# Optimization experiments

Hardware: AMD Instinct MI355X
Metric: run time of the kernel (lower is better)

Reference implementation:

```python
import jax, jax.numpy as jnp
import numpy as np

TOP_K = 2
ROUTED_SCALING = 1.0


def setup_inputs() -> dict:
    key = jax.random.key(0)
    k1, k2, k3, k4 = jax.random.split(key, 4)
    S, B, H = 1024, 2, 1024
    E, FFN = 8, 1408
    return {
        "hidden_states": jax.random.normal(k1, (S, B, H), dtype=jnp.float32),
        "gate_w": jax.random.normal(k2, (E, H), dtype=jnp.float32) * 0.02,
        "w1": jax.random.normal(k3, (E, H, 2 * FFN), dtype=jnp.float32) * 0.02,
        "w2": jax.random.normal(k4, (E, FFN, H), dtype=jnp.float32) * 0.02,
    }


def reference(hidden_states, gate_w, w1, w2):
    # hidden_states: [S, B, H] -> transpose(0,1) as in MoELayer.forward
    x = jnp.transpose(hidden_states, (1, 0, 2))  # [B, S, H]
    B, S, H = x.shape
    E = gate_w.shape[0]
    xt = x.reshape(-1, H)  # [T, H], T = B*S
    T = xt.shape[0]

    # --- TopKGate ('greedy', softmax scoring) ---
    scores = jax.nn.softmax(xt @ gate_w.T, axis=-1)  # [T, E]
    topk_w, topk_idx = jax.lax.top_k(scores, TOP_K)  # [T, K]
    # norm_topk_prob: normalize the top-k weights
    topk_w = topk_w / (jnp.sum(topk_w, axis=-1, keepdims=True) + 1e-20)
    topk_w = topk_w * ROUTED_SCALING

    # Sparse combine weights [T, E] (zero for non-selected experts)
    combine = jnp.zeros((T, E), dtype=xt.dtype)
    combine = combine.at[jnp.arange(T)[:, None], topk_idx].set(topk_w)

    # --- Experts: per-expert swiglu MLP, weighted combine ---
    # Equivalent math to dispatch -> per-expert grouped GEMM -> combine:
    # non-selected experts contribute with weight 0.
    out = jnp.zeros_like(xt)
    for e in range(E):
        h = xt @ w1[e]                      # [T, 2*FFN]
        g, u = jnp.split(h, 2, axis=-1)
        y = (jax.nn.silu(g) * u) @ w2[e]    # [T, H]
        out = out + combine[:, e:e + 1] * y

    out = out.reshape(B, S, H)
    return jnp.transpose(out, (1, 0, 2))  # back to [S, B, H]
```

## Files before the change

kernel.cpp:

```cpp
#include <hip/hip_runtime.h>
#include <hip/hip_bf16.h>

#define S_      1024
#define B_      2
#define H_      1024
#define E_      8
#define FFN_    1408
#define TWO_FFN 2816
#define T_      2048
#define MAXSLOTS 5120
#define NB_CONV 512

typedef float  f32x4 __attribute__((ext_vector_type(4)));
typedef short  s16x8 __attribute__((ext_vector_type(8)));

__device__ __forceinline__ unsigned short f2bf(float f) {
    unsigned u = __float_as_uint(f);
    u += 0x7fffu + ((u >> 16) & 1u);
    return (unsigned short)(u >> 16);
}
__device__ __forceinline__ void async16(const void* g, void* l) {
    __builtin_amdgcn_global_load_lds(
        (const __attribute__((address_space(1))) unsigned int*)(unsigned long long)g,
        (__attribute__((address_space(3))) unsigned int*)(unsigned long long)l,
        16, 0, 0);
}
__device__ __forceinline__ size_t xrow_off(int t) {
    return (size_t)(t & (S_ - 1)) * (B_ * H_) + (size_t)(t >> 10) * H_;
}

__device__ __forceinline__ void stage_b_f32(const float* __restrict__ p, size_t Cs,
                                            unsigned* const bw[4]) {
    float4 v[8];
#pragma unroll
    for (int r = 0; r < 8; r++) v[r] = *(const float4*)(p + (size_t)r * Cs);
#pragma unroll
    for (int jh = 0; jh < 2; jh++) {
        const float4 a0 = v[4 * jh + 0], a1 = v[4 * jh + 1];
        const float4 b0 = v[4 * jh + 2], b1 = v[4 * jh + 3];
        unsigned ua[4], ub[4];
        ua[0] = f2bf(a0.x) | ((unsigned)f2bf(a1.x) << 16);
        ua[1] = f2bf(a0.y) | ((unsigned)f2bf(a1.y) << 16);
        ua[2] = f2bf(a0.z) | ((unsigned)f2bf(a1.z) << 16);
        ua[3] = f2bf(a0.w) | ((unsigned)f2bf(a1.w) << 16);
        ub[0] = f2bf(b0.x) | ((unsigned)f2bf(b1.x) << 16);
        ub[1] = f2bf(b0.y) | ((unsigned)f2bf(b1.y) << 16);
        ub[2] = f2bf(b0.z) | ((unsigned)f2bf(b1.z) << 16);
        ub[3] = f2bf(b0.w) | ((unsigned)f2bf(b1.w) << 16);
#pragma unroll
        for (int i = 0; i < 4; i++) {
            uint2 w; w.x = ua[i]; w.y = ub[i];
            *(uint2*)(bw[i] + 2 * jh) = w;
        }
    }
}

__global__ void k_prep(const float* __restrict__ hs, const float* __restrict__ gw,
                       unsigned short* __restrict__ xb,
                       int* __restrict__ topkI, float* __restrict__ topkW) {
    int cb = blockIdx.x, tid = threadIdx.x;
    int wid = tid >> 6, lane = tid & 63;
    int t = cb * 4 + wid;
    const float* xr = hs + xrow_off(t);
    unsigned short* xo = xb + (size_t)t * H_;
    float acc[E_];
#pragma unroll
    for (int e = 0; e < E_; e++) acc[e] = 0.f;
#pragma unroll
    for (int p = 0; p < 4; p++) {
        int h = p * 256 + lane * 4;
        const float4 v = *(const float4*)(xr + h);
        unsigned short o[4] = { f2bf(v.x), f2bf(v.y), f2bf(v.z), f2bf(v.w) };
        *(uint2*)(xo + h) = *(const uint2*)o;
#pragma unroll
        for (int e = 0; e < E_; e++) {
            const float4 g = *(const float4*)(gw + e * H_ + h);
            acc[e] += v.x * g.x + v.y * g.y + v.z * g.z + v.w * g.w;
        }
    }
#pragma unroll
    for (int e = 0; e < E_; e++)
        for (int off = 32; off > 0; off >>= 1) acc[e] += __shfl_down(acc[e], off);
    if (lane == 0) {
        float l0 = -1e30f, l1 = -1e30f; int i0 = 0, i1 = 0;
#pragma unroll
        for (int e = 0; e < E_; e++) {
            float v = acc[e];
            if (v > l0)      { l1 = l0; i1 = i0; l0 = v; i0 = e; }
            else if (v > l1) { l1 = v;  i1 = e; }
        }
        float p1 = expf(l1 - l0);
        float w0 = 1.f / (1.f + p1);
        float w1s = 1.f - w0;
        topkI[2 * t] = i0; topkI[2 * t + 1] = i1;
        topkW[2 * t] = w0; topkW[2 * t + 1] = w1s;
    }
}

__global__ void k_routeassign(const int* __restrict__ topkI, const float* __restrict__ topkW,
                              int* __restrict__ ctrl, int* __restrict__ perm,
                              int* __restrict__ slotOfTok) {
    __shared__ int s_wcnt[4][E_];
    __shared__ int s_base[E_];
    __shared__ int s_cur[E_];
    int tid = threadIdx.x, wid = tid >> 6, lane = tid & 63;
    int cnt[E_];
#pragma unroll
    for (int j = 0; j < E_; j++) cnt[j] = 0;
    for (int i = tid; i < 2 * T_; i += 256) {
        int e = topkI[i];
#pragma unroll
        for (int j = 0; j < E_; j++) cnt[j] += (e == j);
    }
#pragma unroll
    for (int j = 0; j < E_; j++)
        for (int off = 32; off > 0; off >>= 1) cnt[j] += __shfl_down(cnt[j], off);
    if (lane == 0) {
#pragma unroll
        for (int j = 0; j < E_; j++) s_wcnt[wid][j] = cnt[j];
    }
    __syncthreads();
    if (tid == 0) {
        int b = 0;
        for (int e = 0; e < E_; e++) {
            int n = s_wcnt[0][e] + s_wcnt[1][e] + s_wcnt[2][e] + s_wcnt[3][e];
            int ntile = (n + 127) >> 7;
            s_base[e] = b;
            ctrl[40 + e] = ntile;
            ctrl[48 + e] = b;
            b += ntile * 128;
        }
#pragma unroll
        for (int e = 0; e < E_; e++) s_cur[e] = 0;
    }
    __syncthreads();
    for (int s = tid; s < MAXSLOTS; s += 256) perm[s] = 0;
    __syncthreads();
    for (int t = tid; t < T_; t += 256) {
#pragma unroll
        for (int k = 0; k < 2; k++) {
            int e = topkI[2 * t + k];
            int pos = atomicAdd(&s_cur[e], 1);
            int slot = s_base[e] + pos;
            perm[slot] = t;
            slotOfTok[2 * t + k] = slot;
        }
    }
}

__global__ __launch_bounds__(256) void k_gemm1(
    const unsigned short* __restrict__ xb, const float* __restrict__ w1,
    const int* __restrict__ ctrl, const int* __restrict__ perm,
    unsigned short* __restrict__ A2) {
    int b  = blockIdx.x;
    int p  = ((b >> 7) << 3) | (b & 7);
    int ti = (b >> 3) & 15;
    int e  = p / 22;
    int ct = p - e * 22;
    if (ti >= ctrl[40 + e]) return;
    int slot0 = ctrl[48 + e] + ti * 128;
    __shared__ __align__(16) unsigned short smem[2 * 128 * 64];
    unsigned short* As = smem;
    unsigned short* Bs = smem + 128 * 64;
    int tid = threadIdx.x, wid = tid >> 6, lane = tid & 63;

    const unsigned short* aPtr[4];
    unsigned short* lA[4];
#pragma unroll
    for (int i = 0; i < 4; i++) {
        int c = (wid * 4 + i) * 64 + lane;
        int r = c >> 3;
        int qd = (c & 7) ^ (r & 7);
        int tok = perm[slot0 + r];
        aPtr[i] = xb + (size_t)tok * H_ + qd * 8;
        lA[i] = As + (size_t)c * 8;
    }
    int h1 = tid >> 7, kp = (tid >> 4) & 7, nq = tid & 15;
    int rb = h1 * 64 + nq * 4;
    const float* bsrc = w1 + (size_t)e * (H_ * TWO_FFN)
                        + (h1 ? (FFN_ + ct * 64) : (ct * 64)) + nq * 4
                        + (size_t)(kp * 8) * TWO_FFN;
    unsigned* bw[4];
#pragma unroll
    for (int i = 0; i < 4; i++)
        bw[i] = (unsigned*)Bs + (rb + i) * 32 + ((kp ^ ((rb & 7) + i)) << 2);

    f32x4 acc[4][4];
#pragma unroll
    for (int mi = 0; mi < 4; mi++)
#pragma unroll
        for (int ni = 0; ni < 4; ni++) acc[mi][ni] = (f32x4){0.f, 0.f, 0.f, 0.f};
    int wm = wid & 1, wn = wid >> 1;
    int rowB = wm * 64, colB = wn * 64;
    int sw = (lane & 7) << 3;

    for (int k0 = 0; k0 < H_; k0 += 64) {
#pragma unroll
        for (int i = 0; i < 4; i++) async16(aPtr[i] + k0, lA[i]);
        stage_b_f32(bsrc + (size_t)k0 * TWO_FFN, TWO_FFN, bw);
        __syncthreads();
#pragma unroll
        for (int kk = 0; kk < 64; kk += 32) {
            int kr = (kk + ((lane >> 4) << 3)) ^ sw;
            s16x8 af[4], bf[4];
#pragma unroll
            for (int mi = 0; mi < 4; mi++) af[mi] = *(const s16x8*)&As[(rowB + mi * 16 + (lane & 15)) * 64 + kr];
#pragma unroll
            for (int ni = 0; ni < 4; ni++) bf[ni] = *(const s16x8*)&Bs[(colB + ni * 16 + (lane & 15)) * 64 + kr];
#pragma unroll
            for (int mi = 0; mi < 4; mi++)
#pragma unroll
                for (int ni = 0; ni < 4; ni++)
                    acc[mi][ni] = __builtin_amdgcn_mfma_f32_16x16x32_bf16(af[mi], bf[ni], acc[mi][ni], 0, 0, 0);
        }
        __syncthreads();
    }
    float* upLds = (float*)smem;
    if (wn == 1) {
#pragma unroll
        for (int mi = 0; mi < 4; mi++)
#pragma unroll
            for (int ni = 0; ni < 4; ni++)
#pragma unroll
                for (int r = 0; r < 4; r++) {
                    int m = rowB + mi * 16 + (lane >> 4) * 4 + r;
                    int u = ni * 16 + (lane & 15);
                    upLds[m * 64 + u] = acc[mi][ni][r];
                }
    }
    __syncthreads();
    if (wn == 0) {
#pragma unroll
        for (int mi = 0; mi < 4; mi++)
#pragma unroll
            for (int r = 0; r < 4; r++) {
                int m = rowB + mi * 16 + (lane >> 4) * 4 + r;
                unsigned short* arow = A2 + (size_t)(slot0 + m) * FFN_ + ct * 64;
#pragma unroll
                for (int ni = 0; ni < 4; ni++) {
                    int gl = ni * 16 + (lane & 15);
                    float g = acc[mi][ni][r];
                    float u = upLds[m * 64 + gl];
                    float s = g / (1.f + expf(-g));
                    arow[gl] = f2bf(s * u);
                }
            }
    }
}

__global__ __launch_bounds__(256) void k_gemm2(
    const unsigned short* __restrict__ A2, const float* __restrict__ w2,
    const int* __restrict__ ctrl, unsigned short* __restrict__ Yp) {
    int b  = blockIdx.x;
    int p  = ((b >> 7) << 3) | (b & 7);
    int ti = (b >> 3) & 15;
    int e  = p >> 4;
    int ct = (p >> 1) & 7;
    int ks = p & 1;
    if (ti >= ctrl[40 + e]) return;
    int slot0 = ctrl[48 + e] + ti * 128;
    __shared__ __align__(16) unsigned short As[128 * 64];
    __shared__ __align__(16) unsigned short Bs[128 * 64];
    int tid = threadIdx.x, wid = tid >> 6, lane = tid & 63;

    const unsigned short* aPtr[4];
    unsigned short* lA[4];
#pragma unroll
    for (int i = 0; i < 4; i++) {
        int c = (wid * 4 + i) * 64 + lane;
        int r = c >> 3;
        int qd = (c & 7) ^ (r & 7);
        aPtr[i] = A2 + (size_t)(slot0 + r) * FFN_ + qd * 8;
        lA[i] = As + (size_t)c * 8;
    }
    int h1 = tid >> 7, kp = (tid >> 4) & 7, nq = tid & 15;
    int rb = h1 * 64 + nq * 4;
    const float* bsrc = w2 + (size_t)e * (FFN_ * H_)
                        + ct * 128 + h1 * 64 + nq * 4
                        + (size_t)(kp * 8) * H_;
    unsigned* bw[4];
#pragma unroll
    for (int i = 0; i < 4; i++)
        bw[i] = (unsigned*)Bs + (rb + i) * 32 + ((kp ^ ((rb & 7) + i)) << 2);

    f32x4 acc[4][4];
#pragma unroll
    for (int mi = 0; mi < 4; mi++)
#pragma unroll
        for (int ni = 0; ni < 4; ni++) acc[mi][ni] = (f32x4){0.f, 0.f, 0.f, 0.f};
    int wm = wid & 1, wn = wid >> 1;
    int rowB = wm * 64, colB = wn * 64;
    int sw = (lane & 7) << 3;

    int kbeg = ks * (FFN_ / 2), kend = kbeg + FFN_ / 2;
    for (int k0 = kbeg; k0 < kend; k0 += 64) {
#pragma unroll
        for (int i = 0; i < 4; i++) async16(aPtr[i] + k0, lA[i]);
        stage_b_f32(bsrc + (size_t)k0 * H_, H_, bw);
        __syncthreads();
#pragma unroll
        for (int kk = 0; kk < 64; kk += 32) {
            int kr = (kk + ((lane >> 4) << 3)) ^ sw;
            s16x8 af[4], bf[4];
#pragma unroll
            for (int mi = 0; mi < 4; mi++) af[mi] = *(const s16x8*)&As[(rowB + mi * 16 + (lane & 15)) * 64 + kr];
#pragma unroll
            for (int ni = 0; ni < 4; ni++) bf[ni] = *(const s16x8*)&Bs[(colB + ni * 16 + (lane & 15)) * 64 + kr];
#pragma unroll
            for (int mi = 0; mi < 4; mi++)
#pragma unroll
                for (int ni = 0; ni < 4; ni++)
                    acc[mi][ni] = __builtin_amdgcn_mfma_f32_16x16x32_bf16(af[mi], bf[ni], acc[mi][ni], 0, 0, 0);
        }
        __syncthreads();
    }
    unsigned short* yp = Yp + (size_t)ks * MAXSLOTS * H_;
#pragma unroll
    for (int mi = 0; mi < 4; mi++)
#pragma unroll
        for (int r = 0; r < 4; r++) {
            int m = rowB + mi * 16 + (lane >> 4) * 4 + r;
#pragma unroll
            for (int ni = 0; ni < 4; ni++) {
                int n = colB + ni * 16 + (lane & 15);
                yp[(size_t)(slot0 + m) * H_ + ct * 128 + n] = f2bf(acc[mi][ni][r]);
            }
        }
}

__global__ void k_combine(const unsigned short* __restrict__ Yp, const int* __restrict__ slotOfTok,
                          const float* __restrict__ topkW, float* __restrict__ out) {
    int t = blockIdx.x;
    int h = threadIdx.x * 4;
    int sA = slotOfTok[2 * t], sB = slotOfTok[2 * t + 1];
    float wA = topkW[2 * t],   wB = topkW[2 * t + 1];
    const unsigned short* pA0 = Yp + (size_t)sA * H_ + h;
    const unsigned short* pA1 = Yp + ((size_t)MAXSLOTS + sA) * H_ + h;
    const unsigned short* pB0 = Yp + (size_t)sB * H_ + h;
    const unsigned short* pB1 = Yp + ((size_t)MAXSLOTS + sB) * H_ + h;
    unsigned short a0[4], a1[4], b0[4], b1[4];
    *(uint2*)a0 = *(const uint2*)pA0;
    *(uint2*)a1 = *(const uint2*)pA1;
    *(uint2*)b0 = *(const uint2*)pB0;
    *(uint2*)b1 = *(const uint2*)pB1;
    float4 r;
    float* rp = (float*)&r;
#pragma unroll
    for (int i = 0; i < 4; i++) {
        float av = __uint_as_float(((unsigned)a0[i]) << 16) + __uint_as_float(((unsigned)a1[i]) << 16);
        float bv = __uint_as_float(((unsigned)b0[i]) << 16) + __uint_as_float(((unsigned)b1[i]) << 16);
        rp[i] = wA * av + wB * bv;
    }
    *(float4*)(out + xrow_off(t) + h) = r;
}

extern "C" void kernel_launch(void* const* d_in, const int* in_sizes, int n_in,
                              void* d_out, int out_size, void* d_ws, size_t ws_size,
                              hipStream_t stream) {
    (void)in_sizes; (void)n_in; (void)ws_size; (void)out_size;
    const float* hs = (const float*)d_in[0];
    const float* gw = (const float*)d_in[1];
    const float* w1 = (const float*)d_in[2];
    const float* w2 = (const float*)d_in[3];
    float* out = (float*)d_out;
    char* ws = (char*)d_ws;

    int*            ctrl   = (int*)ws;
    int*            topkI  = (int*)(ws + (16u << 10));
    float*          topkW  = (float*)(ws + (48u << 10));
    int*            perm   = (int*)(ws + (80u << 10));
    int*            slotOfTok = (int*)(ws + (144u << 10));
    unsigned short* xb    = (unsigned short*)(ws + (1ull  << 20));
    unsigned short* A2    = (unsigned short*)(ws + (8ull  << 20));
    unsigned short* Yp    = (unsigned short*)(ws + (24ull << 20));

    k_prep<<<NB_CONV, 256, 0, stream>>>(hs, gw, xb, topkI, topkW);
    k_routeassign<<<1, 256, 0, stream>>>(topkI, topkW, ctrl, perm, slotOfTok);
    k_gemm1<<<dim3(22 * 128), 256, 0, stream>>>(xb, w1, ctrl, perm, A2);
    k_gemm2<<<dim3(16 * 128), 256, 0, stream>>>(A2, w2, ctrl, Yp);
    k_combine<<<2048, 256, 0, stream>>>(Yp, slotOfTok, topkW, out);
}
```

Before: 303.3 us.

## Double-buffer LDS tiles and prefetch weights in registers in both expert GEMMs

Both grouped GEMM kernels now use two LDS buffers for the A and B tiles. The next A tile is loaded asynchronously and the next fp32 weight tile is held in registers while the MFMAs run on the current tile. This removes one barrier per K step and overlaps global loads with compute. B staging is also rewritten to pack pairs with the hardware bf16 conversion and write one 16-byte store per row. The cost is twice the LDS per block and more live registers, which may reduce occupancy.

Measured after the change: 273.9 us. 1.11x faster.

```diff
diff --git a/kernel.cpp b/kernel.cpp
--- a/kernel.cpp
+++ b/kernel.cpp
@@ -10,6 +10,7 @@
 #define T_      2048
 #define MAXSLOTS 5120
 #define NB_CONV 512
+#define TSZ     (128 * 64)
 
 typedef float  f32x4 __attribute__((ext_vector_type(4)));
 typedef short  s16x8 __attribute__((ext_vector_type(8)));
@@ -18,6 +19,10 @@
     unsigned u = __float_as_uint(f);
     u += 0x7fffu + ((u >> 16) & 1u);
     return (unsigned short)(u >> 16);
+}
+__device__ __forceinline__ unsigned pk2(float a, float b) {
+    __hip_bfloat162 h = __float22bfloat162_rn(make_float2(a, b));
+    unsigned u; __builtin_memcpy(&u, &h, 4); return u;
 }
 __device__ __forceinline__ void async16(const void* g, void* l) {
     __builtin_amdgcn_global_load_lds(
@@ -29,29 +34,39 @@
     return (size_t)(t & (S_ - 1)) * (B_ * H_) + (size_t)(t >> 10) * H_;
 }
 
-__device__ __forceinline__ void stage_b_f32(const float* __restrict__ p, size_t Cs,
-                                            unsigned* const bw[4]) {
-    float4 v[8];
-#pragma unroll
-    for (int r = 0; r < 8; r++) v[r] = *(const float4*)(p + (size_t)r * Cs);
-#pragma unroll
-    for (int jh = 0; jh < 2; jh++) {
-        const float4 a0 = v[4 * jh + 0], a1 = v[4 * jh + 1];
-        const float4 b0 = v[4 * jh + 2], b1 = v[4 * jh + 3];
-        unsigned ua[4], ub[4];
-        ua[0] = f2bf(a0.x) | ((unsigned)f2bf(a1.x) << 16);
-        ua[1] = f2bf(a0.y) | ((unsigned)f2bf(a1.y) << 16);
-        ua[2] = f2bf(a0.z) | ((unsigned)f2bf(a1.z) << 16);
-        ua[3] = f2bf(a0.w) | ((unsigned)f2bf(a1.w) << 16);
-        ub[0] = f2bf(b0.x) | ((unsigned)f2bf(b1.x) << 16);
-        ub[1] = f2bf(b0.y) | ((unsigned)f2bf(b1.y) << 16);
-        ub[2] = f2bf(b0.z) | ((unsigned)f2bf(b1.z) << 16);
-        ub[3] = f2bf(b0.w) | ((unsigned)f2bf(b1.w) << 16);
-#pragma unroll
-        for (int i = 0; i < 4; i++) {
-            uint2 w; w.x = ua[i]; w.y = ub[i];
-            *(uint2*)(bw[i] + 2 * jh) = w;
-        }
+__device__ __forceinline__ void load8(f32x4 v[8], const float* __restrict__ p, size_t C) {
+#pragma unroll
+    for (int j = 0; j < 8; j++) v[j] = *(const f32x4*)(p + (size_t)j * C);
+}
+__device__ __forceinline__ void stage_wr(const f32x4 v[8], unsigned* __restrict__ base,
+                                         const int off[4]) {
+#pragma unroll
+    for (int i = 0; i < 4; i++) {
+        uint4 q;
+        q.x = pk2(v[0][i], v[1][i]);
+        q.y = pk2(v[2][i], v[3][i]);
+        q.z = pk2(v[4][i], v[5][i]);
+        q.w = pk2(v[6][i], v[7][i]);
+        *(uint4*)(base + off[i]) = q;
+    }
+}
+__device__ __forceinline__ void mfma_step(const unsigned short* __restrict__ As,
+                                          const unsigned short* __restrict__ Bs,
+                                          f32x4 acc[4][4], int rowB, int colB, int lane) {
+    int sw = (lane & 7) << 3;
+#pragma unroll
+    for (int kk = 0; kk < 64; kk += 32) {
+        int kr = (kk + ((lane >> 4) << 3)) ^ sw;
+        s16x8 af[4], bf[4];
+#pragma unroll
+        for (int mi = 0; mi < 4; mi++) af[mi] = *(const s16x8*)&As[(rowB + mi * 16 + (lane & 15)) * 64 + kr];
+#pragma unroll
+        for (int ni = 0; ni < 4; ni++) bf[ni] = *(const s16x8*)&Bs[(colB + ni * 16 + (lane & 15)) * 64 + kr];
+#pragma unroll
+        for (int mi = 0; mi < 4; mi++)
+#pragma unroll
+            for (int ni = 0; ni < 4; ni++)
+                acc[mi][ni] = __builtin_amdgcn_mfma_f32_16x16x32_bf16(af[mi], bf[ni], acc[mi][ni], 0, 0, 0);
     }
 }
 
@@ -159,13 +174,12 @@
     int ct = p - e * 22;
     if (ti >= ctrl[40 + e]) return;
     int slot0 = ctrl[48 + e] + ti * 128;
-    __shared__ __align__(16) unsigned short smem[2 * 128 * 64];
-    unsigned short* As = smem;
-    unsigned short* Bs = smem + 128 * 64;
+    __shared__ __align__(16) unsigned short As[2 * TSZ];
+    __shared__ __align__(16) unsigned short Bs[2 * TSZ];
     int tid = threadIdx.x, wid = tid >> 6, lane = tid & 63;
 
     const unsigned short* aPtr[4];
-    unsigned short* lA[4];
+    int lAoff[4];
 #pragma unroll
     for (int i = 0; i < 4; i++) {
         int c = (wid * 4 + i) * 64 + lane;
@@ -173,17 +187,17 @@
         int qd = (c & 7) ^ (r & 7);
         int tok = perm[slot0 + r];
         aPtr[i] = xb + (size_t)tok * H_ + qd * 8;
-        lA[i] = As + (size_t)c * 8;
+        lAoff[i] = c * 8;
     }
     int h1 = tid >> 7, kp = (tid >> 4) & 7, nq = tid & 15;
     int rb = h1 * 64 + nq * 4;
     const float* bsrc = w1 + (size_t)e * (H_ * TWO_FFN)
                         + (h1 ? (FFN_ + ct * 64) : (ct * 64)) + nq * 4
                         + (size_t)(kp * 8) * TWO_FFN;
-    unsigned* bw[4];
+    int bwOff[4];
 #pragma unroll
     for (int i = 0; i < 4; i++)
-        bw[i] = (unsigned*)Bs + (rb + i) * 32 + ((kp ^ ((rb & 7) + i)) << 2);
+        bwOff[i] = (rb + i) * 32 + ((kp ^ ((rb + i) & 7)) << 2);
 
     f32x4 acc[4][4];
 #pragma unroll
@@ -192,30 +206,34 @@
         for (int ni = 0; ni < 4; ni++) acc[mi][ni] = (f32x4){0.f, 0.f, 0.f, 0.f};
     int wm = wid & 1, wn = wid >> 1;
     int rowB = wm * 64, colB = wn * 64;
-    int sw = (lane & 7) << 3;
-
-    for (int k0 = 0; k0 < H_; k0 += 64) {
-#pragma unroll
-        for (int i = 0; i < 4; i++) async16(aPtr[i] + k0, lA[i]);
-        stage_b_f32(bsrc + (size_t)k0 * TWO_FFN, TWO_FFN, bw);
+
+    f32x4 bv[8];
+    load8(bv, bsrc, TWO_FFN);
+    stage_wr(bv, (unsigned*)Bs, bwOff);
+#pragma unroll
+    for (int i = 0; i < 4; i++) async16(aPtr[i], As + lAoff[i]);
+    load8(bv, bsrc + (size_t)64 * TWO_FFN, TWO_FFN);
+#pragma unroll
+    for (int i = 0; i < 4; i++) async16(aPtr[i] + 64, As + TSZ + lAoff[i]);
+    __syncthreads();
+
+    int cur = 0;
+#pragma unroll 1
+    for (int s = 0; s < 16; s++) {
+        mfma_step(As + cur * TSZ, Bs + cur * TSZ, acc, rowB, colB, lane);
+        if (s == 15) break;
+        stage_wr(bv, (unsigned*)(Bs + (cur ^ 1) * TSZ), bwOff);
         __syncthreads();
-#pragma unroll
-        for (int kk = 0; kk < 64; kk += 32) {
-            int kr = (kk + ((lane >> 4) << 3)) ^ sw;
-            s16x8 af[4], bf[4];
-#pragma unroll
-            for (int mi = 0; mi < 4; mi++) af[mi] = *(const s16x8*)&As[(rowB + mi * 16 + (lane & 15)) * 64 + kr];
-#pragma unroll
-            for (int ni = 0; ni < 4; ni++) bf[ni] = *(const s16x8*)&Bs[(colB + ni * 16 + (lane & 15)) * 64 + kr];
-#pragma unroll
-            for (int mi = 0; mi < 4; mi++)
-#pragma unroll
-                for (int ni = 0; ni < 4; ni++)
-                    acc[mi][ni] = __builtin_amdgcn_mfma_f32_16x16x32_bf16(af[mi], bf[ni], acc[mi][ni], 0, 0, 0);
-        }
-        __syncthreads();
-    }
-    float* upLds = (float*)smem;
+        if (s < 14) {
+            size_t k2 = (size_t)(s + 2) * 64;
+#pragma unroll
+            for (int i = 0; i < 4; i++) async16(aPtr[i] + k2, As + cur * TSZ + lAoff[i]);
+            load8(bv, bsrc + k2 * TWO_FFN, TWO_FFN);
+        }
+        cur ^= 1;
+    }
+    __syncthreads();
+    float* upLds = (float*)As;
     if (wn == 1) {
 #pragma unroll
         for (int mi = 0; mi < 4; mi++)
@@ -259,29 +277,30 @@
     int ks = p & 1;
     if (ti >= ctrl[40 + e]) return;
     int slot0 = ctrl[48 + e] + ti * 128;
-    __shared__ __align__(16) unsigned short As[128 * 64];
-    __shared__ __align__(16) unsigned short Bs[128 * 64];
+    __shared__ __align__(16) unsigned short As[2 * TSZ];
+    __shared__ __align__(16) unsigned short Bs[2 * TSZ];
     int tid = threadIdx.x, wid = tid >> 6, lane = tid & 63;
 
     const unsigned short* aPtr[4];
-    unsigned short* lA[4];
+    int lAoff[4];
 #pragma unroll
     for (int i = 0; i < 4; i++) {
         int c = (wid * 4 + i) * 64 + lane;
         int r = c >> 3;
         int qd = (c & 7) ^ (r & 7);
         aPtr[i] = A2 + (size_t)(slot0 + r) * FFN_ + qd * 8;
-        lA[i] = As + (size_t)c * 8;
+        lAoff[i] = c * 8;
     }
     int h1 = tid >> 7, kp = (tid >> 4) & 7, nq = tid & 15;
     int rb = h1 * 64 + nq * 4;
+    int kbeg = ks * (FFN_ / 2);
     const float* bsrc = w2 + (size_t)e * (FFN_ * H_)
                         + ct * 128 + h1 * 64 + nq * 4
-                        + (size_t)(kp * 8) * H_;
-    unsigned* bw[4];
+                        + (size_t)(kp * 8 + kbeg) * H_;
+    int bwOff[4];
 #pragma unroll
     for (int i = 0; i < 4; i++)
-        bw[i] = (unsigned*)Bs + (rb + i) * 32 + ((kp ^ ((rb & 7) + i)) << 2);
+        bwOff[i] = (rb + i) * 32 + ((kp ^ ((rb + i) & 7)) << 2);
 
     f32x4 acc[4][4];
 #pragma unroll
@@ -290,29 +309,31 @@
         for (int ni = 0; ni < 4; ni++) acc[mi][ni] = (f32x4){0.f, 0.f, 0.f, 0.f};
     int wm = wid & 1, wn = wid >> 1;
     int rowB = wm * 64, colB = wn * 64;
-    int sw = (lane & 7) << 3;
-
-    int kbeg = ks * (FFN_ / 2), kend = kbeg + FFN_ / 2;
-    for (int k0 = kbeg; k0 < kend; k0 += 64) {
-#pragma unroll
-        for (int i = 0; i < 4; i++) async16(aPtr[i] + k0, lA[i]);
-        stage_b_f32(bsrc + (size_t)k0 * H_, H_, bw);
+
+    f32x4 bv[8];
+    load8(bv, bsrc, H_);
+    stage_wr(bv, (unsigned*)Bs, bwOff);
+#pragma unroll
+    for (int i = 0; i < 4; i++) async16(aPtr[i] + kbeg, As + lAoff[i]);
+    load8(bv, bsrc + (size_t)64 * H_, H_);
+#pragma unroll
+    for (int i = 0; i < 4; i++) async16(aPtr[i] + kbeg + 64, As + TSZ + lAoff[i]);
+    __syncthreads();
+
+    int cur = 0;
+#pragma unroll 1
+    for (int s = 0; s < 11; s++) {
+        mfma_step(As + cur * TSZ, Bs + cur * TSZ, acc, rowB, colB, lane);
+        if (s == 10) break;
+        stage_wr(bv, (unsigned*)(Bs + (cur ^ 1) * TSZ), bwOff);
         __syncthreads();
-#pragma unroll
-        for (int kk = 0; kk < 64; kk += 32) {
-            int kr = (kk + ((lane >> 4) << 3)) ^ sw;
-            s16x8 af[4], bf[4];
-#pragma unroll
-            for (int mi = 0; mi < 4; mi++) af[mi] = *(const s16x8*)&As[(rowB + mi * 16 + (lane & 15)) * 64 + kr];
-#pragma unroll
-            for (int ni = 0; ni < 4; ni++) bf[ni] = *(const s16x8*)&Bs[(colB + ni * 16 + (lane & 15)) * 64 + kr];
-#pragma unroll
-            for (int mi = 0; mi < 4; mi++)
-#pragma unroll
-                for (int ni = 0; ni < 4; ni++)
-                    acc[mi][ni] = __builtin_amdgcn_mfma_f32_16x16x32_bf16(af[mi], bf[ni], acc[mi][ni], 0, 0, 0);
-        }
-        __syncthreads();
+        if (s < 9) {
+            size_t k2 = (size_t)(s + 2) * 64;
+#pragma unroll
+            for (int i = 0; i < 4; i++) async16(aPtr[i] + kbeg + k2, As + cur * TSZ + lAoff[i]);
+            load8(bv, bsrc + k2 * H_, H_);
+        }
+        cur ^= 1;
     }
     unsigned short* yp = Yp + (size_t)ks * MAXSLOTS * H_;
 #pragma unroll
```
